# Optimization experiments

Measured on AMD Instinct MI355X. Metric: run time of the kernel, lower is better.

## Reference

```python
import jax, jax.numpy as jnp
import numpy as np

# SRU cell math (sru library v2.x, has_skip_term=False, identity activation):
#   U = x @ W  ->  split into (u0, u1, u2), each [L, B, H]
#   f_t = sigmoid(u1_t + v_f * c_{t-1} + b_f)
#   r_t = sigmoid(u2_t + v_r * c_{t-1} + b_r)
#   c_t = f_t * c_{t-1} + (1 - f_t) * u0_t
#   h_t = r_t * c_t            (no skip term, identity activation)

L, B, D, H, OUT = 512, 128, 128, 512, 5


def sru_layer(x, W, vc, b):
    # x: [L, B, Din]; W: [Din, 3H]; vc: [2H]; b: [2H]
    h = W.shape[1] // 3
    U = jnp.einsum('lbd,dk->lbk', x, W)          # [L, B, 3H]
    u0, u1, u2 = jnp.split(U, 3, axis=-1)
    vf, vr = vc[:h], vc[h:]
    bf, br = b[:h], b[h:]

    def step(c, u):
        u0t, u1t, u2t = u
        f = jax.nn.sigmoid(u1t + vf * c + bf)
        r = jax.nn.sigmoid(u2t + vr * c + br)
        c_new = f * c + (1.0 - f) * u0t
        return c_new, r * c_new

    c0 = jnp.zeros((x.shape[1], h), dtype=x.dtype)
    _, hs = jax.lax.scan(step, c0, (u0, u1, u2))  # hs: [L, B, H]
    return hs


def setup_inputs() -> dict:
    key = jax.random.key(0)
    ks = jax.random.split(key, 9)
    s_in = 1.0 / np.sqrt(D)
    s_h = 1.0 / np.sqrt(H)
    return {
        'x': jax.random.normal(ks[0], (L, B, D), jnp.float32),
        'W0': jax.random.normal(ks[1], (D, 3 * H), jnp.float32) * s_in,
        'v0': jax.random.normal(ks[2], (2 * H,), jnp.float32) * s_h,
        'b0': jnp.zeros((2 * H,), jnp.float32),
        'W1': jax.random.normal(ks[3], (H, 3 * H), jnp.float32) * s_h,
        'v1': jax.random.normal(ks[4], (2 * H,), jnp.float32) * s_h,
        'b1': jnp.zeros((2 * H,), jnp.float32),
        'fc_w': jax.random.normal(ks[5], (OUT, H), jnp.float32) * s_h,
        'fc_b': jnp.zeros((OUT,), jnp.float32),
    }


def reference(x, W0, v0, b0, W1, v1, b1, fc_w, fc_b):
    h1 = sru_layer(x, W0, v0, b0)    # [L, B, H]
    h2 = sru_layer(h1, W1, v1, b1)   # [L, B, H]
    # fc on last timestep
    return h2[-1] @ fc_w.T + fc_b    # [B, OUT]
```

## Files before the change

kernel.cpp:

```cpp
#include <hip/hip_runtime.h>
#include <math.h>

#define L_SEQ 512
#define BATCH 128
#define DIN   128
#define HID   512
#define NOUT  5
#define NSTR  1536

typedef unsigned short u16;
typedef unsigned int   u32;
typedef __attribute__((ext_vector_type(8))) short short8;
typedef __attribute__((ext_vector_type(4))) float f32x4;

__device__ __forceinline__ u16 f2bf(float x) {
  u32 u = __float_as_uint(x);
  return (u16)((u + 0x7fffu + ((u >> 16) & 1u)) >> 16);
}
__device__ __forceinline__ float bf2f(u16 s) {
  return __uint_as_float(((u32)s) << 16);
}
__device__ __forceinline__ void gload16(const void* g, void* l) {
  __builtin_amdgcn_global_load_lds(
      (const __attribute__((address_space(1))) u32*)g,
      (__attribute__((address_space(3))) u32*)l, 16, 0, 0);
}

struct GArgs {
  const u16* Ah; const u16* Al;
  const u16* Bh; const u16* Bl;
  float* C;
  int K;
  int NBX;
};

__global__ __launch_bounds__(256, 4)
void gemm_dual(GArgs g0, int nblk0, GArgs g1) {
  const bool first = (int)blockIdx.x < nblk0;
  const GArgs g = first ? g0 : g1;
  int bid = first ? (int)blockIdx.x : (int)blockIdx.x - nblk0;
  const int nsub = first ? nblk0 : (int)gridDim.x - nblk0;
  if ((nsub & 7) == 0) {
    const int cpx = nsub >> 3;
    bid = (bid & 7) * cpx + (bid >> 3);
  }
  const int K = g.K;

  __shared__ u16 sAh[4096], sAl[4096], sBh[4096], sBl[4096];

  const int bx = bid % g.NBX;
  const int by = bid / g.NBX;
  const int tid = threadIdx.x;
  const int wid = tid >> 6, lane = tid & 63;

  const int srow = tid >> 2;
  const int sw = (tid & 3) ^ ((srow >> 1) & 3);
  const size_t aoff0 = (size_t)(by * 128 + srow) * K + sw * 8;
  const size_t aoff1 = aoff0 + (size_t)64 * K;
  const size_t boff0 = (size_t)(bx * 128 + srow) * K + sw * 8;
  const size_t boff1 = boff0 + (size_t)64 * K;
  const int d0 = wid * 512;
  const int d1 = 2048 + wid * 512;

  const int wm = wid >> 1, wn = wid & 1;
  const int frow = lane & 15, fsl = lane >> 4;
  int offA[4], offB[4];
#pragma unroll
  for (int i = 0; i < 4; ++i) {
    const int ra = wm * 64 + i * 16 + frow;
    offA[i] = ra * 32 + ((fsl ^ ((ra >> 1) & 3)) * 8);
    const int rb = wn * 64 + i * 16 + frow;
    offB[i] = rb * 32 + ((fsl ^ ((rb >> 1) & 3)) * 8);
  }

  f32x4 acc[4][4];
#pragma unroll
  for (int i = 0; i < 4; ++i)
#pragma unroll
    for (int j = 0; j < 4; ++j)
#pragma unroll
      for (int q = 0; q < 4; ++q) acc[i][j][q] = 0.f;

  for (int k0 = 0; k0 < K; k0 += 32) {
    __syncthreads();
    gload16(g.Ah + aoff0 + k0, &sAh[d0]);
    gload16(g.Ah + aoff1 + k0, &sAh[d1]);
    gload16(g.Al + aoff0 + k0, &sAl[d0]);
    gload16(g.Al + aoff1 + k0, &sAl[d1]);
    gload16(g.Bh + boff0 + k0, &sBh[d0]);
    gload16(g.Bh + boff1 + k0, &sBh[d1]);
    gload16(g.Bl + boff0 + k0, &sBl[d0]);
    gload16(g.Bl + boff1 + k0, &sBl[d1]);
    __syncthreads();

    short8 bh[4], bl[4];
#pragma unroll
    for (int j = 0; j < 4; ++j) {
      bh[j] = *(const short8*)&sBh[offB[j]];
      bl[j] = *(const short8*)&sBl[offB[j]];
    }
#pragma unroll
    for (int i = 0; i < 4; ++i) {
      const short8 ah = *(const short8*)&sAh[offA[i]];
      const short8 al = *(const short8*)&sAl[offA[i]];
#pragma unroll
      for (int j = 0; j < 4; ++j) {
        acc[i][j] = __builtin_amdgcn_mfma_f32_16x16x32_bf16(ah, bh[j], acc[i][j], 0, 0, 0);
        acc[i][j] = __builtin_amdgcn_mfma_f32_16x16x32_bf16(ah, bl[j], acc[i][j], 0, 0, 0);
        acc[i][j] = __builtin_amdgcn_mfma_f32_16x16x32_bf16(al, bh[j], acc[i][j], 0, 0, 0);
      }
    }
  }

  const int crow0 = by * 128 + wm * 64 + (lane >> 4) * 4;
  const int ccol0 = bx * 128 + wn * 64 + (lane & 15);
#pragma unroll
  for (int i = 0; i < 4; ++i)
#pragma unroll
    for (int j = 0; j < 4; ++j) {
      float* cp = g.C + (size_t)(crow0 + i * 16) * NSTR + ccol0 + j * 16;
#pragma unroll
      for (int q = 0; q < 4; ++q) cp[(size_t)q * NSTR] = acc[i][j][q];
    }
}

__global__ __launch_bounds__(256)
void split4_f32(const float* __restrict__ in, u16* __restrict__ hi,
                u16* __restrict__ lo, int n4) {
  const int i = blockIdx.x * 256 + threadIdx.x;
  if (i >= n4) return;
  const float4 v = ((const float4*)in)[i];
  u16 h0 = f2bf(v.x), h1 = f2bf(v.y), h2 = f2bf(v.z), h3 = f2bf(v.w);
  u16 l0 = f2bf(v.x - bf2f(h0)), l1 = f2bf(v.y - bf2f(h1));
  u16 l2 = f2bf(v.z - bf2f(h2)), l3 = f2bf(v.w - bf2f(h3));
  uint2 hp, lp;
  hp.x = (u32)h0 | ((u32)h1 << 16); hp.y = (u32)h2 | ((u32)h3 << 16);
  lp.x = (u32)l0 | ((u32)l1 << 16); lp.y = (u32)l2 | ((u32)l3 << 16);
  ((uint2*)hi)[i] = hp;
  ((uint2*)lo)[i] = lp;
}

__global__ __launch_bounds__(256)
void split_w_t(const float* __restrict__ W, u16* __restrict__ Th,
               u16* __restrict__ Tl, int K, int N) {
  const int idx = blockIdx.x * 256 + threadIdx.x;
  if (idx >= K * N) return;
  const int k = idx / N, n = idx - k * N;
  const float x = W[idx];
  const u16 h = f2bf(x);
  Th[(size_t)n * K + k] = h;
  Tl[(size_t)n * K + k] = f2bf(x - bf2f(h));
}

__device__ __forceinline__ float sig(float x) { return 1.f / (1.f + __expf(-x)); }

__device__ __forceinline__
void scan0_body(int j, const float* __restrict__ U, const float* __restrict__ v,
                const float* __restrict__ bias, u16* __restrict__ h1h,
                u16* __restrict__ h1l, float* __restrict__ cstate, int Tc, int init) {
  const int b = j >> 9, h = j & (HID - 1);
  const float vf = v[h], vr = v[HID + h];
  const float bf = bias[h], br = bias[HID + h];

  const float* p = U + (size_t)b * NSTR + h;
  const size_t sT = (size_t)BATCH * NSTR;
  u16* ph = h1h + (size_t)b * HID + h;
  u16* pl = h1l + (size_t)b * HID + h;
  const size_t sH = (size_t)BATCH * HID;

  float c = init ? 0.f : cstate[j];
  float cu[24];
#pragma unroll
  for (int q = 0; q < 8; ++q) {
    cu[3 * q + 0] = p[q * sT];
    cu[3 * q + 1] = p[q * sT + HID];
    cu[3 * q + 2] = p[q * sT + 2 * HID];
  }
  const int NG = Tc >> 3;
  for (int g = 0; g < NG; ++g) {
    float nx[24];
    const bool has = (g + 1 < NG);
    if (has) {
      const float* pn = p + 8 * sT;
#pragma unroll
      for (int q = 0; q < 8; ++q) {
        nx[3 * q + 0] = pn[q * sT];
        nx[3 * q + 1] = pn[q * sT + HID];
        nx[3 * q + 2] = pn[q * sT + 2 * HID];
      }
    }
#pragma unroll
    for (int q = 0; q < 8; ++q) {
      const float u0 = cu[3 * q], u1 = cu[3 * q + 1], u2 = cu[3 * q + 2];
      const float f = sig(u1 + vf * c + bf);
      const float r = sig(u2 + vr * c + br);
      c = f * c + (1.f - f) * u0;
      const float hv = r * c;
      const u16 hh = f2bf(hv);
      ph[(size_t)(g * 8 + q) * sH] = hh;
      pl[(size_t)(g * 8 + q) * sH] = f2bf(hv - bf2f(hh));
    }
    p += 8 * sT;
    if (has) {
#pragma unroll
      for (int i = 0; i < 24; ++i) cu[i] = nx[i];
    }
  }
  cstate[j] = c;
}

__device__ __forceinline__
void scan1_body(int j, const float* __restrict__ U, const float* __restrict__ v,
                const float* __restrict__ bias, float* __restrict__ cstate,
                float* __restrict__ hlast, int Tc, int lastT, int init) {
  const int b = j >> 9, h = j & (HID - 1);
  const float vf = v[h], vr = v[HID + h];
  const float bf = bias[h], br = bias[HID + h];

  const float* p = U + (size_t)b * NSTR + h;
  const size_t sT = (size_t)BATCH * NSTR;

  float c = init ? 0.f : cstate[j];
  float cu[16];
#pragma unroll
  for (int q = 0; q < 8; ++q) {
    cu[2 * q + 0] = p[q * sT];
    cu[2 * q + 1] = p[q * sT + HID];
  }
  const int NG = Tc >> 3;
  for (int g = 0; g < NG; ++g) {
    float nx[16];
    const bool has = (g + 1 < NG);
    if (has) {
      const float* pn = p + 8 * sT;
#pragma unroll
      for (int q = 0; q < 8; ++q) {
        nx[2 * q + 0] = pn[q * sT];
        nx[2 * q + 1] = pn[q * sT + HID];
      }
    }
#pragma unroll
    for (int q = 0; q < 8; ++q) {
      const float u0 = cu[2 * q], u1 = cu[2 * q + 1];
      const float f = sig(u1 + vf * c + bf);
      const float cn = f * c + (1.f - f) * u0;
      if (g * 8 + q == lastT) {
        const float u2 = p[q * sT + 2 * HID];
        const float r = sig(u2 + vr * c + br);
        hlast[j] = r * cn;
      }
      c = cn;
    }
    p += 8 * sT;
    if (has) {
#pragma unroll
      for (int i = 0; i < 16; ++i) cu[i] = nx[i];
    }
  }
  cstate[j] = c;
}

__global__ __launch_bounds__(256)
void sru_scan0(const float* __restrict__ U, const float* __restrict__ v,
               const float* __restrict__ bias, u16* __restrict__ h1h,
               u16* __restrict__ h1l, float* __restrict__ cstate, int Tc, int init) {
  scan0_body(blockIdx.x * 256 + threadIdx.x, U, v, bias, h1h, h1l, cstate, Tc, init);
}

__global__ __launch_bounds__(256)
void scan_dual(const float* __restrict__ U1, const float* __restrict__ v1,
               const float* __restrict__ b1, float* __restrict__ c1,
               float* __restrict__ h2, int lastT, int init1,
               const float* __restrict__ U0n, const float* __restrict__ v0,
               const float* __restrict__ b0, u16* __restrict__ h1h,
               u16* __restrict__ h1l, float* __restrict__ c0, int Tc) {
  const int nb1 = (BATCH * HID) / 256;
  if ((int)blockIdx.x < nb1) {
    scan1_body(blockIdx.x * 256 + threadIdx.x, U1, v1, b1, c1, h2, Tc, lastT, init1);
  } else {
    scan0_body((blockIdx.x - nb1) * 256 + threadIdx.x, U0n, v0, b0, h1h, h1l, c0, Tc, 0);
  }
}

__global__ __launch_bounds__(256)
void fc_head(const float* __restrict__ h, const float* __restrict__ w,
             const float* __restrict__ bias, float* __restrict__ out) {
  const int gid = blockIdx.x * 256 + threadIdx.x;
  const int wv = gid >> 6, lane = threadIdx.x & 63;
  if (wv >= BATCH * NOUT) return;
  const int b = wv / NOUT, o = wv % NOUT;
  float s = 0.f;
#pragma unroll
  for (int k = lane; k < HID; k += 64)
    s += h[(size_t)b * HID + k] * w[(size_t)o * HID + k];
#pragma unroll
  for (int off = 32; off > 0; off >>= 1) s += __shfl_down(s, off);
  if (lane == 0) out[(size_t)b * NOUT + o] = s + bias[o];
}

extern "C" void kernel_launch(void* const* d_in, const int* in_sizes, int n_in,
                              void* d_out, int out_size, void* d_ws, size_t ws_size,
                              hipStream_t stream) {
  const float* x   = (const float*)d_in[0];
  const float* W0  = (const float*)d_in[1];
  const float* v0  = (const float*)d_in[2];
  const float* b0  = (const float*)d_in[3];
  const float* W1  = (const float*)d_in[4];
  const float* v1  = (const float*)d_in[5];
  const float* b1  = (const float*)d_in[6];
  const float* fcw = (const float*)d_in[7];
  const float* fcb = (const float*)d_in[8];
  float* out = (float*)d_out;

  const size_t nX  = (size_t)L_SEQ * BATCH * DIN;
  const size_t nW0 = (size_t)DIN * NSTR;
  const size_t nW1 = (size_t)HID * NSTR;

  int Tc = 64;
  for (;;) {
    size_t f32e = 3 * (size_t)Tc * BATCH * NSTR + 3 * (size_t)BATCH * HID;
    size_t u16e = 2 * nX + 4 * (size_t)Tc * BATCH * HID + 2 * nW0 + 2 * nW1;
    if (f32e * 4 + u16e * 2 + 1024 <= ws_size || Tc <= 8) break;
    Tc >>= 1;
  }
  const int NC = L_SEQ / Tc;
  const int Mc = Tc * BATCH;

  float* U1c   = (float*)d_ws;
  float* U0a   = U1c + (size_t)Mc * NSTR;
  float* U0b   = U0a + (size_t)Mc * NSTR;
  float* c0    = U0b + (size_t)Mc * NSTR;
  float* c1    = c0 + (size_t)BATCH * HID;
  float* h2    = c1 + (size_t)BATCH * HID;
  u16* xs_h    = (u16*)(h2 + (size_t)BATCH * HID);
  u16* xs_l    = xs_h + nX;
  u16* h1h_a   = xs_l + nX;
  u16* h1l_a   = h1h_a + (size_t)Mc * HID;
  u16* h1h_b   = h1l_a + (size_t)Mc * HID;
  u16* h1l_b   = h1h_b + (size_t)Mc * HID;
  u16* w0t_h   = h1l_b + (size_t)Mc * HID;
  u16* w0t_l   = w0t_h + nW0;
  u16* w1t_h   = w0t_l + nW0;
  u16* w1t_l   = w1t_h + nW1;

  float* U0[2]  = {U0a, U0b};
  u16* h1h[2]   = {h1h_a, h1h_b};
  u16* h1l[2]   = {h1l_a, h1l_b};

  const int rows   = Mc / 128;
  const int fcGrid = (BATCH * NOUT * 64 + 255) / 256;

  split4_f32<<<(int)(nX / 4 + 255) / 256, 256, 0, stream>>>(x, xs_h, xs_l, (int)(nX / 4));
  split_w_t<<<(int)(nW0 + 255) / 256, 256, 0, stream>>>(W0, w0t_h, w0t_l, DIN, NSTR);
  split_w_t<<<(int)(nW1 + 255) / 256, 256, 0, stream>>>(W1, w1t_h, w1t_l, HID, NSTR);

  {
    GArgs ga = {xs_h, xs_l, w0t_h, w0t_l, U0[0], DIN, 12};
    gemm_dual<<<rows * 12, 256, 0, stream>>>(ga, rows * 12, ga);
    sru_scan0<<<(BATCH * HID) / 256, 256, 0, stream>>>(U0[0], v0, b0,
                                                       h1h[0], h1l[0], c0, Tc, 1);
  }

  for (int ch = 0; ch < NC; ++ch) {
    const bool last = (ch == NC - 1);
    const int cur = ch & 1, nxt = cur ^ 1;
    const int nbx1 = last ? 12 : 8;
    const int nb0 = rows * nbx1;

    GArgs g1 = {h1h[cur], h1l[cur], w1t_h, w1t_l, U1c, HID, nbx1};
    GArgs g0n = g1;
    int nb1 = 0;
    if (!last) {
      const size_t xoff = (size_t)(ch + 1) * Mc * DIN;
      g0n = GArgs{xs_h + xoff, xs_l + xoff, w0t_h, w0t_l, U0[nxt], DIN, 12};
      nb1 = rows * 12;
    }
    gemm_dual<<<nb0 + nb1, 256, 0, stream>>>(g1, nb0, g0n);

    scan_dual<<<last ? 256 : 512, 256, 0, stream>>>(
        U1c, v1, b1, c1, h2, last ? Tc - 1 : -1, ch == 0,
        U0[nxt], v0, b0, h1h[nxt], h1l[nxt], c0, Tc);
  }
  fc_head<<<fcGrid, 256, 0, stream>>>(h2, fcw, fcb, out);
}
```

Before: 602.6 us.

## Run layer-1 scan of previous chunk inside GEMM launch as rider blocks

Restructures the per-chunk schedule. The layer-1 recurrence for chunk ch-1 now runs as extra 'rider' blocks inside the GEMM launch for chunk ch, using a float4-vectorised scan over a double-buffered U1 holding only the f/u0 columns (stride 1024). The layer-0 scan becomes its own kernel, and a final layer-1 scan computes the last-timestep output. This overlaps the latency-bound layer-1 scan with GEMM compute and removes the layer-1 gate columns from intermediate chunks, at the cost of extra launches per chunk and a serial final scan.

```diff
diff --git a/kernel.cpp b/kernel.cpp
--- a/kernel.cpp
+++ b/kernel.cpp
@@ -25,6 +25,59 @@
       (const __attribute__((address_space(1))) u32*)g,
       (__attribute__((address_space(3))) u32*)l, 16, 0, 0);
 }
+__device__ __forceinline__ float sig(float x) { return 1.f / (1.f + __expf(-x)); }
+
+__device__ void scan1_vec4(int idx, const float* __restrict__ U, int S,
+                           const float* __restrict__ v, const float* __restrict__ bias,
+                           float* __restrict__ c1, int Tc, int init) {
+  const int j4 = idx * 4;
+  const int b = j4 >> 9, h = j4 & (HID - 1);
+  const float4 vf = *(const float4*)(v + h);
+  const float4 bf = *(const float4*)(bias + h);
+  const float* p = U + (size_t)b * S + h;
+  const size_t sT = (size_t)BATCH * S;
+
+  float4 c;
+  if (init) { c.x = c.y = c.z = c.w = 0.f; } else { c = *(const float4*)(c1 + j4); }
+
+  float4 u0g[4], u1g[4];
+#pragma unroll
+  for (int q = 0; q < 4; ++q) {
+    u0g[q] = *(const float4*)(p + q * sT);
+    u1g[q] = *(const float4*)(p + q * sT + HID);
+  }
+  const int NG = Tc >> 2;
+  for (int g = 0; g < NG; ++g) {
+    float4 n0[4], n1[4];
+    const bool has = (g + 1 < NG);
+    if (has) {
+      const float* pn = p + 4 * sT;
+#pragma unroll
+      for (int q = 0; q < 4; ++q) {
+        n0[q] = *(const float4*)(pn + q * sT);
+        n1[q] = *(const float4*)(pn + q * sT + HID);
+      }
+    }
+#pragma unroll
+    for (int q = 0; q < 4; ++q) {
+      float4 f;
+      f.x = sig(u1g[q].x + vf.x * c.x + bf.x);
+      f.y = sig(u1g[q].y + vf.y * c.y + bf.y);
+      f.z = sig(u1g[q].z + vf.z * c.z + bf.z);
+      f.w = sig(u1g[q].w + vf.w * c.w + bf.w);
+      c.x = f.x * c.x + (1.f - f.x) * u0g[q].x;
+      c.y = f.y * c.y + (1.f - f.y) * u0g[q].y;
+      c.z = f.z * c.z + (1.f - f.z) * u0g[q].z;
+      c.w = f.w * c.w + (1.f - f.w) * u0g[q].w;
+    }
+    p += 4 * sT;
+    if (has) {
+#pragma unroll
+      for (int q = 0; q < 4; ++q) { u0g[q] = n0[q]; u1g[q] = n1[q]; }
+    }
+  }
+  *(float4*)(c1 + j4) = c;
+}
 
 struct GArgs {
   const u16* Ah; const u16* Al;
@@ -32,14 +85,22 @@
   float* C;
   int K;
   int NBX;
+  int Cs;
 };
 
 __global__ __launch_bounds__(256, 4)
-void gemm_dual(GArgs g0, int nblk0, GArgs g1) {
-  const bool first = (int)blockIdx.x < nblk0;
+void gemm_tri(GArgs g0, int nb0, GArgs g1, int nb1,
+              const float* sU, int sS, const float* sv, const float* sb,
+              float* sc1, int sTc, int sInit, int nrider) {
+  if ((int)blockIdx.x < nrider) {
+    scan1_vec4((int)blockIdx.x * 256 + threadIdx.x, sU, sS, sv, sb, sc1, sTc, sInit);
+    return;
+  }
+  const int bxg = (int)blockIdx.x - nrider;
+  const bool first = bxg < nb0;
   const GArgs g = first ? g0 : g1;
-  int bid = first ? (int)blockIdx.x : (int)blockIdx.x - nblk0;
-  const int nsub = first ? nblk0 : (int)gridDim.x - nblk0;
+  int bid = first ? bxg : bxg - nb0;
+  const int nsub = first ? nb0 : nb1;
   if ((nsub & 7) == 0) {
     const int cpx = nsub >> 3;
     bid = (bid & 7) * cpx + (bid >> 3);
@@ -118,9 +179,9 @@
   for (int i = 0; i < 4; ++i)
 #pragma unroll
     for (int j = 0; j < 4; ++j) {
-      float* cp = g.C + (size_t)(crow0 + i * 16) * NSTR + ccol0 + j * 16;
-#pragma unroll
-      for (int q = 0; q < 4; ++q) cp[(size_t)q * NSTR] = acc[i][j][q];
+      float* cp = g.C + (size_t)(crow0 + i * 16) * g.Cs + ccol0 + j * 16;
+#pragma unroll
+      for (int q = 0; q < 4; ++q) cp[(size_t)q * g.Cs] = acc[i][j][q];
     }
 }
 
@@ -152,12 +213,11 @@
   Tl[(size_t)n * K + k] = f2bf(x - bf2f(h));
 }
 
-__device__ __forceinline__ float sig(float x) { return 1.f / (1.f + __expf(-x)); }
-
-__device__ __forceinline__
-void scan0_body(int j, const float* __restrict__ U, const float* __restrict__ v,
-                const float* __restrict__ bias, u16* __restrict__ h1h,
-                u16* __restrict__ h1l, float* __restrict__ cstate, int Tc, int init) {
+__global__ __launch_bounds__(256)
+void sru_scan0(const float* __restrict__ U, const float* __restrict__ v,
+               const float* __restrict__ bias, u16* __restrict__ h1h,
+               u16* __restrict__ h1l, float* __restrict__ cstate, int Tc, int init) {
+  const int j = blockIdx.x * 256 + threadIdx.x;
   const int b = j >> 9, h = j & (HID - 1);
   const float vf = v[h], vr = v[HID + h];
   const float bf = bias[h], br = bias[HID + h];
@@ -209,10 +269,11 @@
   cstate[j] = c;
 }
 
-__device__ __forceinline__
-void scan1_body(int j, const float* __restrict__ U, const float* __restrict__ v,
-                const float* __restrict__ bias, float* __restrict__ cstate,
-                float* __restrict__ hlast, int Tc, int lastT, int init) {
+__global__ __launch_bounds__(256)
+void sru_scan1(const float* __restrict__ U, const float* __restrict__ v,
+               const float* __restrict__ bias, float* __restrict__ cstate,
+               float* __restrict__ hlast, int Tc, int lastT, int init) {
+  const int j = blockIdx.x * 256 + threadIdx.x;
   const int b = j >> 9, h = j & (HID - 1);
   const float vf = v[h], vr = v[HID + h];
   const float bf = bias[h], br = bias[HID + h];
@@ -258,28 +319,6 @@
     }
   }
   cstate[j] = c;
-}
-
-__global__ __launch_bounds__(256)
-void sru_scan0(const float* __restrict__ U, const float* __restrict__ v,
-               const float* __restrict__ bias, u16* __restrict__ h1h,
-               u16* __restrict__ h1l, float* __restrict__ cstate, int Tc, int init) {
-  scan0_body(blockIdx.x * 256 + threadIdx.x, U, v, bias, h1h, h1l, cstate, Tc, init);
-}
-
-__global__ __launch_bounds__(256)
-void scan_dual(const float* __restrict__ U1, const float* __restrict__ v1,
-               const float* __restrict__ b1, float* __restrict__ c1,
-               float* __restrict__ h2, int lastT, int init1,
-               const float* __restrict__ U0n, const float* __restrict__ v0,
-               const float* __restrict__ b0, u16* __restrict__ h1h,
-               u16* __restrict__ h1l, float* __restrict__ c0, int Tc) {
-  const int nb1 = (BATCH * HID) / 256;
-  if ((int)blockIdx.x < nb1) {
-    scan1_body(blockIdx.x * 256 + threadIdx.x, U1, v1, b1, c1, h2, Tc, lastT, init1);
-  } else {
-    scan0_body((blockIdx.x - nb1) * 256 + threadIdx.x, U0n, v0, b0, h1h, h1l, c0, Tc, 0);
-  }
 }
 
 __global__ __launch_bounds__(256)
@@ -318,7 +357,8 @@
 
   int Tc = 64;
   for (;;) {
-    size_t f32e = 3 * (size_t)Tc * BATCH * NSTR + 3 * (size_t)BATCH * HID;
+    size_t f32e = (size_t)Tc * BATCH * NSTR + 2 * (size_t)Tc * BATCH * 1024 +
+                  3 * (size_t)BATCH * HID;
     size_t u16e = 2 * nX + 4 * (size_t)Tc * BATCH * HID + 2 * nW0 + 2 * nW1;
     if (f32e * 4 + u16e * 2 + 1024 <= ws_size || Tc <= 8) break;
     Tc >>= 1;
@@ -326,10 +366,10 @@
   const int NC = L_SEQ / Tc;
   const int Mc = Tc * BATCH;
 
-  float* U1c   = (float*)d_ws;
-  float* U0a   = U1c + (size_t)Mc * NSTR;
-  float* U0b   = U0a + (size_t)Mc * NSTR;
-  float* c0    = U0b + (size_t)Mc * NSTR;
+  float* U0    = (float*)d_ws;
+  float* U1a   = U0  + (size_t)Mc * NSTR;
+  float* U1b   = U1a + (size_t)Mc * 1024;
+  float* c0    = U1b + (size_t)Mc * 1024;
   float* c1    = c0 + (size_t)BATCH * HID;
   float* h2    = c1 + (size_t)BATCH * HID;
   u16* xs_h    = (u16*)(h2 + (size_t)BATCH * HID);
@@ -343,43 +383,52 @@
   u16* w1t_h   = w0t_l + nW0;
   u16* w1t_l   = w1t_h + nW1;
 
-  float* U0[2]  = {U0a, U0b};
-  u16* h1h[2]   = {h1h_a, h1h_b};
-  u16* h1l[2]   = {h1l_a, h1l_b};
+  float* U1[2] = {U1a, U1b};
+  u16* h1h[2]  = {h1h_a, h1h_b};
+  u16* h1l[2]  = {h1l_a, h1l_b};
 
   const int rows   = Mc / 128;
   const int fcGrid = (BATCH * NOUT * 64 + 255) / 256;
+  const int NRIDER = (BATCH * HID) / (256 * 4);
 
   split4_f32<<<(int)(nX / 4 + 255) / 256, 256, 0, stream>>>(x, xs_h, xs_l, (int)(nX / 4));
   split_w_t<<<(int)(nW0 + 255) / 256, 256, 0, stream>>>(W0, w0t_h, w0t_l, DIN, NSTR);
   split_w_t<<<(int)(nW1 + 255) / 256, 256, 0, stream>>>(W1, w1t_h, w1t_l, HID, NSTR);
 
   {
-    GArgs ga = {xs_h, xs_l, w0t_h, w0t_l, U0[0], DIN, 12};
-    gemm_dual<<<rows * 12, 256, 0, stream>>>(ga, rows * 12, ga);
-    sru_scan0<<<(BATCH * HID) / 256, 256, 0, stream>>>(U0[0], v0, b0,
+    GArgs ga = {xs_h, xs_l, w0t_h, w0t_l, U0, DIN, 12, NSTR};
+    gemm_tri<<<rows * 12, 256, 0, stream>>>(ga, rows * 12, ga, 0,
+                                            nullptr, 0, nullptr, nullptr,
+                                            nullptr, 0, 0, 0);
+    sru_scan0<<<(BATCH * HID) / 256, 256, 0, stream>>>(U0, v0, b0,
                                                        h1h[0], h1l[0], c0, Tc, 1);
   }
 
   for (int ch = 0; ch < NC; ++ch) {
     const bool last = (ch == NC - 1);
     const int cur = ch & 1, nxt = cur ^ 1;
-    const int nbx1 = last ? 12 : 8;
-    const int nb0 = rows * nbx1;
-
-    GArgs g1 = {h1h[cur], h1l[cur], w1t_h, w1t_l, U1c, HID, nbx1};
+
+    GArgs g1 = {h1h[cur], h1l[cur], w1t_h, w1t_l,
+                last ? U0 : U1[cur], HID, last ? 12 : 8, last ? NSTR : 1024};
+    const int nb0 = rows * (last ? 12 : 8);
     GArgs g0n = g1;
     int nb1 = 0;
     if (!last) {
       const size_t xoff = (size_t)(ch + 1) * Mc * DIN;
-      g0n = GArgs{xs_h + xoff, xs_l + xoff, w0t_h, w0t_l, U0[nxt], DIN, 12};
+      g0n = GArgs{xs_h + xoff, xs_l + xoff, w0t_h, w0t_l, U0, DIN, 12, NSTR};
       nb1 = rows * 12;
     }
-    gemm_dual<<<nb0 + nb1, 256, 0, stream>>>(g1, nb0, g0n);
-
-    scan_dual<<<last ? 256 : 512, 256, 0, stream>>>(
-        U1c, v1, b1, c1, h2, last ? Tc - 1 : -1, ch == 0,
-        U0[nxt], v0, b0, h1h[nxt], h1l[nxt], c0, Tc);
-  }
+    const int nr = (ch > 0) ? NRIDER : 0;
+    gemm_tri<<<nr + nb0 + nb1, 256, 0, stream>>>(
+        g1, nb0, g0n, nb1,
+        (ch > 0) ? U1[(ch - 1) & 1] : nullptr, 1024, v1, b1, c1, Tc,
+        (ch == 1) ? 1 : 0, nr);
+
+    if (!last)
+      sru_scan0<<<(BATCH * HID) / 256, 256, 0, stream>>>(U0, v0, b0,
+                                                         h1h[nxt], h1l[nxt], c0, Tc, 0);
+  }
+  sru_scan1<<<(BATCH * HID) / 256, 256, 0, stream>>>(
+      U0, v1, b1, c1, h2, Tc, Tc - 1, (NC == 1) ? 1 : 0);
   fc_head<<<fcGrid, 256, 0, stream>>>(h2, fcw, fcb, out);
 }
```

New measurement: 608.7 us. Within noise of the previous version (+1.0%).
